# Kernel tuning notes

Hardware: AMD Instinct MI355X
Metric: run time of the kernel (lower is better)

Reference implementation:

```python
import jax, jax.numpy as jnp
import numpy as np

EPS = 1e-5  # BatchNorm eps (torch default)
K = 16      # num_neighbors


def _bn(x, gamma, beta, axes):
    # training-mode BatchNorm (biased variance), channel axis = 1
    mu = x.mean(axes, keepdims=True)
    var = x.var(axes, keepdims=True)
    shp = [1] * x.ndim
    shp[1] = -1
    return (x - mu) * jax.lax.rsqrt(var + EPS) * gamma.reshape(shp) + beta.reshape(shp)


def setup_inputs() -> dict:
    key = jax.random.key(0)
    ks = jax.random.split(key, 6)
    B, C, N, E = 4, 3, 4096, 256
    s = lambda k_, shp, fan: jax.random.normal(k_, shp, jnp.float32) * np.float32(1.0 / np.sqrt(fan))
    return {
        "x": jax.random.normal(ks[0], (B, C, N), jnp.float32),
        "g1": jnp.ones((C,), jnp.float32), "b1": jnp.zeros((C,), jnp.float32),
        "W1": s(ks[1], (E, C), C), "bw1": jnp.zeros((E,), jnp.float32),
        "g2a": jnp.ones((C,), jnp.float32), "b2a": jnp.zeros((C,), jnp.float32),
        "W2a": s(ks[2], (E, C), C),
        "g2b": jnp.ones((E,), jnp.float32), "b2b": jnp.zeros((E,), jnp.float32),
        "W2b": s(ks[3], (E, E), E),
        "Wf": s(ks[4], (E, 2 * E), 2 * E), "bf": jnp.zeros((E,), jnp.float32),
    }


def reference(x, g1, b1, W1, bw1, g2a, b2a, W2a, g2b, b2b, W2b, Wf, bf):
    B, C, N = x.shape
    xn = _bn(x, g1, b1, (0, 2))                               # BatchNorm1d
    point_emb = jnp.einsum('ec,bcn->ben', W1, xn) + bw1[None, :, None]  # conv1 (1x1)
    # dist = -||xi - xj||; torch topk(dist, largest=False) picks the K LARGEST
    # distances. Squared distance is monotone in the norm, so top_k on d2 gives
    # identical indices without materializing [B,3,N,N].
    x2 = jnp.sum(xn * xn, axis=1)                             # [B,N]
    d2 = x2[:, :, None] + x2[:, None, :] - 2.0 * jnp.einsum('bcn,bcm->bnm', xn, xn)
    _, idx = jax.lax.top_k(d2, min(K, N))                     # [B,N,K]
    idx = idx[:, :, 1:]                                       # original loop skips index 0
    gathered = jax.vmap(lambda xb, ib: xb[:, ib])(xn, idx)    # [B,C,N,K-1]
    neigh = gathered - xn[:, :, :, None]                      # edge features
    h = _bn(neigh, g2a, b2a, (0, 2, 3))                       # BatchNorm2d(Cin)
    h = jnp.einsum('ec,bcnk->benk', W2a, h)                   # 1x1 conv, no bias
    h = jax.nn.gelu(_bn(h, g2b, b2b, (0, 2, 3)), approximate=False)
    h = jnp.einsum('fe,benk->bfnk', W2b, h)                   # 1x1 conv, no bias
    neigh_emb = h.max(-1)                                     # max over neighbors
    feat = jnp.concatenate([point_emb, neigh_emb], axis=1)    # [B,2E,N]
    return jnp.einsum('of,bfn->bon', Wf, feat) + bf[None, :, None]
```

## Files before the change

### kernel.cpp

```cpp
#include <hip/hip_runtime.h>
#include <float.h>
#include <math.h>

#define EPS 1e-5f
constexpr int B = 4, C = 3, N = 4096, E = 256;
constexpr int KNN = 15;
constexpr int BN_ = B * N;
constexpr int P = 8;
constexpr int SR  = 264;
constexpr int SRF = 520;

typedef short bf8 __attribute__((ext_vector_type(8)));
typedef float f4  __attribute__((ext_vector_type(4)));

static __device__ __forceinline__ unsigned short f2bf(float f) {
    union { float f; unsigned int u; } v; v.f = f;
    unsigned int r = v.u + 0x7FFFu + ((v.u >> 16) & 1u);
    return (unsigned short)(r >> 16);
}
static __device__ __forceinline__ bf8 ld_bf8(const unsigned short* p) {
    return *(const bf8*)p;
}
static __device__ __forceinline__ float gelu_t(float v) {
    float z = v * fmaf(v * v, 0.07135482f, 1.59576912f);
    float r = __builtin_amdgcn_rcpf(1.f + __expf(z));
    return fmaf(-v, r, v);
}

__global__ void bn1_stats(const float* __restrict__ x, float* __restrict__ bn1) {
    int c = blockIdx.x, t = threadIdx.x;
    float s = 0.f, ss = 0.f;
    for (int i4 = t; i4 < BN_ / 4; i4 += 256) {
        int b = i4 >> 10, n4 = i4 & 1023;
        float4 v = ((const float4*)(x + (b * C + c) * N))[n4];
        s += v.x + v.y + v.z + v.w;
        ss += v.x * v.x + v.y * v.y + v.z * v.z + v.w * v.w;
    }
    __shared__ float rs_[256], rss_[256];
    rs_[t] = s; rss_[t] = ss; __syncthreads();
    for (int w = 128; w > 0; w >>= 1) {
        if (t < w) { rs_[t] += rs_[t + w]; rss_[t] += rss_[t + w]; }
        __syncthreads();
    }
    if (t == 0) {
        float mu = rs_[0] / (float)BN_;
        float var = rss_[0] / (float)BN_ - mu * mu;
        bn1[c] = mu; bn1[3 + c] = rsqrtf(var + EPS);
    }
}

__global__ void compute_xn_cvt(const float* __restrict__ x,
                               const float* __restrict__ g1,
                               const float* __restrict__ b1,
                               const float* __restrict__ bn1,
                               float4* __restrict__ xn4,
                               const float* __restrict__ W2b, const float* __restrict__ Wf,
                               unsigned short* __restrict__ w2b_t, unsigned short* __restrict__ wf_t) {
    int blk = blockIdx.x;
    if (blk < BN_ / 256) {
        int i = blk * 256 + threadIdx.x;
        int b = i >> 12, n = i & (N - 1);
        float v[3];
        #pragma unroll
        for (int c = 0; c < C; c++)
            v[c] = (x[(b * C + c) * N + n] - bn1[c]) * bn1[3 + c] * g1[c] + b1[c];
        float4 o; o.x = v[0]; o.y = v[1]; o.z = v[2];
        o.w = v[0] * v[0] + v[1] * v[1] + v[2] * v[2];
        xn4[i] = o;
        return;
    }
    int ch = (blk - BN_ / 256) * 256 + threadIdx.x;
    if (ch < 8192) {
        int lane = ch & 63, kb = (ch >> 6) & 7, ft16 = ch >> 9;
        int row = ft16 * 16 + (lane & 15);
        int col = kb * 32 + (lane >> 4) * 8;
        #pragma unroll
        for (int j = 0; j < 8; j++)
            w2b_t[ch * 8 + j] = f2bf(W2b[row * 256 + col + j]);
    } else {
        int c2 = ch - 8192;
        int lane = c2 & 63, kb = (c2 >> 6) & 15, ot = c2 >> 10;
        int row = ot * 16 + (lane & 15);
        int col = kb * 32 + (lane >> 4) * 8;
        #pragma unroll
        for (int j = 0; j < 8; j++)
            wf_t[c2 * 8 + j] = f2bf(Wf[row * 512 + col + j]);
    }
}

__global__ void __launch_bounds__(256, 4) knn_kernel(const float4* __restrict__ xn4,
                                                     unsigned short* __restrict__ idxout,
                                                     float* __restrict__ S9) {
    __shared__ float smom[4][15][9];
    int w = threadIdx.x >> 6, lane = threadIdx.x & 63;
    int i = blockIdx.x * 4 + w;
    int b = i >> 12, n = i & (N - 1);
    const float4* xb = xn4 + b * N;
    float4 qv = xb[n];
    float d[64];
    #pragma unroll
    for (int s = 0; s < 64; s++) {
        float4 p = xb[s * 64 + lane];
        d[s] = qv.w + p.w - 2.f * (qv.x * p.x + qv.y * p.y + qv.z * p.z);
    }
    float cm[8];
    #pragma unroll
    for (int c = 0; c < 8; c++) {
        float v = d[c * 8];
        #pragma unroll
        for (int s = 1; s < 8; s++) v = fmaxf(v, d[c * 8 + s]);
        cm[c] = v;
    }
    float bv = cm[0];
    #pragma unroll
    for (int c = 1; c < 8; c++) bv = fmaxf(bv, cm[c]);

    int myj = 0;
    for (int r = 0; r < 16; r++) {
        float wv = bv;
        #pragma unroll
        for (int off = 32; off > 0; off >>= 1)
            wv = fmaxf(wv, __shfl_xor(wv, off));
        unsigned long long msk = __ballot(bv == wv);
        int wl = __ffsll(msk) - 1;
        int gi = 0;
        if (lane == wl) {
            int cstar = 0; bool got = false;
            #pragma unroll
            for (int c = 0; c < 8; c++) {
                bool h = !got && (cm[c] == bv);
                cstar = h ? c : cstar;
                got = got || h;
            }
            int slot = 0;
            #pragma unroll
            for (int c = 0; c < 8; c++) {
                if (c == cstar) {
                    bool g2 = false;
                    #pragma unroll
                    for (int s = 0; s < 8; s++) {
                        bool h = !g2 && (d[c * 8 + s] == bv);
                        slot = h ? (c * 8 + s) : slot;
                        g2 = g2 || h;
                    }
                    #pragma unroll
                    for (int s = 0; s < 8; s++)
                        d[c * 8 + s] = (c * 8 + s == slot) ? -FLT_MAX : d[c * 8 + s];
                    float v = d[c * 8];
                    #pragma unroll
                    for (int s = 1; s < 8; s++) v = fmaxf(v, d[c * 8 + s]);
                    cm[c] = v;
                }
            }
            bv = cm[0];
            #pragma unroll
            for (int c = 1; c < 8; c++) bv = fmaxf(bv, cm[c]);
            gi = slot * 64 + lane;
        }
        int g = __shfl(gi, wl);
        if (lane == r - 1) myj = g;
    }

    bool act = lane < 15;
    if (act) idxout[i * KNN + lane] = (unsigned short)myj;
    float4 pj = xb[act ? myj : n];
    float v0 = pj.x - qv.x, v1 = pj.y - qv.y, v2 = pj.z - qv.z;
    if (act) {
        float* mm = smom[w][lane];
        mm[0] = v0; mm[1] = v1; mm[2] = v2;
        mm[3] = v0 * v0; mm[4] = v1 * v1; mm[5] = v2 * v2;
        mm[6] = v0 * v1; mm[7] = v0 * v2; mm[8] = v1 * v2;
    }
    __syncthreads();
    int t = threadIdx.x;
    if (t < 36) {
        int wsel = t / 9, j = t % 9;
        float a = 0.f;
        #pragma unroll
        for (int u = 0; u < 15; u++) a += smom[wsel][u][j];
        atomicAdd(&S9[((blockIdx.x * 4 + wsel) & 63) * 9 + j], a);
    }
}

__global__ void finalize_stats(const float* __restrict__ S9,
                               const float* __restrict__ g2a, const float* __restrict__ b2a,
                               const float* __restrict__ W2a,
                               const float* __restrict__ g2b, const float* __restrict__ b2b,
                               float* __restrict__ ab, float4* __restrict__ wsb) {
    const float cnt = (float)(BN_ * KNN);
    __shared__ float S[9];
    __shared__ float alpha[3], beta[3], mu[3], Ehh[3][3];
    int t = threadIdx.x;
    if (t < 9) {
        float a = 0.f;
        for (int u = 0; u < 64; u++) a += S9[u * 9 + t];
        S[t] = a;
    }
    __syncthreads();
    if (t == 0) {
        float m[3];
        float s2[3][3];
        s2[0][0] = S[3]; s2[1][1] = S[4]; s2[2][2] = S[5];
        s2[0][1] = s2[1][0] = S[6]; s2[0][2] = s2[2][0] = S[7]; s2[1][2] = s2[2][1] = S[8];
        for (int c = 0; c < 3; c++) {
            m[c] = S[c] / cnt;
            float var = s2[c][c] / cnt - m[c] * m[c];
            alpha[c] = g2a[c] * rsqrtf(var + EPS);
            beta[c]  = b2a[c] - m[c] * alpha[c];
            mu[c] = m[c];
            ab[c] = alpha[c]; ab[3 + c] = beta[c];
        }
        for (int c = 0; c < 3; c++)
            for (int cc = 0; cc < 3; cc++)
                Ehh[c][cc] = alpha[c] * alpha[cc] * (s2[c][cc] / cnt)
                           + alpha[c] * beta[cc] * m[c]
                           + beta[c] * alpha[cc] * m[cc]
                           + beta[c] * beta[cc];
    }
    __syncthreads();
    int e = t;
    float wv[3], Eh[3];
    for (int c = 0; c < 3; c++) { wv[c] = W2a[e * 3 + c]; Eh[c] = alpha[c] * mu[c] + beta[c]; }
    float mean = wv[0] * Eh[0] + wv[1] * Eh[1] + wv[2] * Eh[2];
    float m2 = 0.f;
    for (int c = 0; c < 3; c++)
        for (int cc = 0; cc < 3; cc++) m2 += wv[c] * wv[cc] * Ehh[c][cc];
    float var = m2 - mean * mean;
    float s = g2b[e] * rsqrtf(var + EPS);
    float4 o;
    o.x = wv[0] * s; o.y = wv[1] * s; o.z = wv[2] * s; o.w = b2b[e] - mean * s;
    wsb[e] = o;
}

__global__ void __launch_bounds__(512, 4) fused_final(
        const float4* __restrict__ xn4, const unsigned short* __restrict__ idx,
        const float* __restrict__ ab,
        const float4* __restrict__ wsb,
        const unsigned short* __restrict__ w2b_t,
        const float* __restrict__ W1, const float* __restrict__ bw1,
        const unsigned short* __restrict__ wf_t, const float* __restrict__ bfv,
        float* __restrict__ out) {
    __shared__ __align__(16) unsigned short hh_bf[128 * SR];
    __shared__ __align__(16) unsigned short feat_bf[8 * SRF];
    __shared__ __align__(16) float4 hhat4[P][16];
    int i0 = blockIdx.x * P;
    int t = threadIdx.x;
    int b = i0 >> 12, n0 = i0 & (N - 1);
    const float4* xb = xn4 + b * N;

    if (t < P * KNN) {
        int p = t / KNN, k = t % KNN;
        int j = idx[(i0 + p) * KNN + k];
        float4 pj = xb[j];
        float4 pn = xb[n0 + p];
        float4 h;
        h.x = ab[0] * (pj.x - pn.x) + ab[3];
        h.y = ab[1] * (pj.y - pn.y) + ab[4];
        h.z = ab[2] * (pj.z - pn.z) + ab[5];
        h.w = 0.f;
        hhat4[p][k] = h;
    }
    __syncthreads();

    {
        int e = t & 255;
        int ph = t >> 8;
        float4 w4 = wsb[e];
        #pragma unroll
        for (int pp = 0; pp < 4; pp++) {
            int p = ph * 4 + pp;
            float g0 = 0.f;
            #pragma unroll
            for (int k = 0; k < KNN; k++) {
                float4 hv = hhat4[p][k];
                float v = fmaf(w4.x, hv.x, fmaf(w4.y, hv.y, fmaf(w4.z, hv.z, w4.w)));
                float g = gelu_t(v);
                hh_bf[(16 * p + k) * SR + e] = f2bf(g);
                if (k == 0) g0 = g;
            }
            hh_bf[(16 * p + 15) * SR + e] = f2bf(g0);
            float4 pv = xb[n0 + p];
            feat_bf[p * SRF + e] = f2bf(bw1[e] + W1[e * 3] * pv.x
                       + W1[e * 3 + 1] * pv.y + W1[e * 3 + 2] * pv.z);
        }
    }
    __syncthreads();

    int w = t >> 6, lane = t & 63;
    int m = lane & 15, q = lane >> 4;

    {
        #pragma unroll
        for (int f = 0; f < 2; f++) {
            int ft = w * 2 + f;
            bf8 a[8];
            #pragma unroll
            for (int kb = 0; kb < 8; kb++)
                a[kb] = ld_bf8(w2b_t + ft * 4096 + kb * 512 + lane * 8);
            #pragma unroll 1
            for (int pr = 0; pr < 4; pr++) {
                bf8 hfr[2][8];
                #pragma unroll
                for (int pi = 0; pi < 2; pi++)
                    #pragma unroll
                    for (int kb = 0; kb < 8; kb++)
                        hfr[pi][kb] = ld_bf8(&hh_bf[(16 * (pr * 2 + pi) + m) * SR + kb * 32 + q * 8]);
                #pragma unroll
                for (int pi = 0; pi < 2; pi++) {
                    f4 acc = {0.f, 0.f, 0.f, 0.f};
                    #pragma unroll
                    for (int kb = 0; kb < 8; kb++)
                        acc = __builtin_amdgcn_mfma_f32_16x16x32_bf16(hfr[pi][kb], a[kb], acc, 0, 0, 0);
                    float mx = fmaxf(fmaxf(acc[0], acc[1]), fmaxf(acc[2], acc[3]));
                    mx = fmaxf(mx, __shfl_xor(mx, 16));
                    mx = fmaxf(mx, __shfl_xor(mx, 32));
                    if (lane < 16)
                        feat_bf[(pr * 2 + pi) * SRF + E + ft * 16 + lane] = f2bf(mx);
                }
            }
        }
    }
    __syncthreads();

    {
        bf8 fb[16];
        #pragma unroll
        for (int kb = 0; kb < 16; kb++)
            fb[kb] = ld_bf8(&feat_bf[(m & 7) * SRF + kb * 32 + q * 8]);
        #pragma unroll
        for (int o2 = 0; o2 < 2; o2++) {
            int ot = w * 2 + o2;
            f4 acc = {0.f, 0.f, 0.f, 0.f};
            #pragma unroll
            for (int kb = 0; kb < 16; kb++) {
                bf8 a = ld_bf8(wf_t + ot * 8192 + kb * 512 + lane * 8);
                acc = __builtin_amdgcn_mfma_f32_16x16x32_bf16(a, fb[kb], acc, 0, 0, 0);
            }
            if (m < P) {
                int o0 = ot * 16 + 4 * q;
                out[(b * E + o0 + 0) * N + n0 + m] = acc[0] + bfv[o0 + 0];
                out[(b * E + o0 + 1) * N + n0 + m] = acc[1] + bfv[o0 + 1];
                out[(b * E + o0 + 2) * N + n0 + m] = acc[2] + bfv[o0 + 2];
                out[(b * E + o0 + 3) * N + n0 + m] = acc[3] + bfv[o0 + 3];
            }
        }
    }
}

extern "C" void kernel_launch(void* const* d_in, const int* in_sizes, int n_in,
                              void* d_out, int out_size, void* d_ws, size_t ws_size,
                              hipStream_t stream) {
    (void)in_sizes; (void)n_in; (void)out_size; (void)ws_size;
    const float* x   = (const float*)d_in[0];
    const float* g1  = (const float*)d_in[1];
    const float* b1  = (const float*)d_in[2];
    const float* W1  = (const float*)d_in[3];
    const float* bw1 = (const float*)d_in[4];
    const float* g2a = (const float*)d_in[5];
    const float* b2a = (const float*)d_in[6];
    const float* W2a = (const float*)d_in[7];
    const float* g2b = (const float*)d_in[8];
    const float* b2b = (const float*)d_in[9];
    const float* W2b = (const float*)d_in[10];
    const float* Wf  = (const float*)d_in[11];
    const float* bfv = (const float*)d_in[12];
    float* out = (float*)d_out;

    char* ws = (char*)d_ws;
    size_t off = 0;
    auto alloc = [&](size_t bytes) { size_t o = off; off = (off + bytes + 255) & ~(size_t)255; return o; };
    float4* xn4           = (float4*)(ws + alloc(sizeof(float4) * BN_));
    unsigned short* idx   = (unsigned short*)(ws + alloc(sizeof(unsigned short) * BN_ * KNN));
    float* bn1            = (float*)(ws + alloc(sizeof(float) * 8));
    float* S9             = (float*)(ws + alloc(sizeof(float) * 64 * 9));
    float* ab             = (float*)(ws + alloc(sizeof(float) * 8));
    float4* wsb           = (float4*)(ws + alloc(sizeof(float4) * E));
    unsigned short* w2bt  = (unsigned short*)(ws + alloc(sizeof(unsigned short) * E * E));
    unsigned short* wft   = (unsigned short*)(ws + alloc(sizeof(unsigned short) * E * 2 * E));

    hipMemsetAsync(S9, 0, sizeof(float) * 64 * 9, stream);

    bn1_stats<<<C, 256, 0, stream>>>(x, bn1);
    compute_xn_cvt<<<BN_ / 256 + (8192 + 16384) / 256, 256, 0, stream>>>(
        x, g1, b1, bn1, xn4, W2b, Wf, w2bt, wft);
    knn_kernel<<<BN_ / 4, 256, 0, stream>>>(xn4, idx, S9);
    finalize_stats<<<1, 256, 0, stream>>>(S9, g2a, b2a, W2a, g2b, b2b, ab, wsb);
    fused_final<<<BN_ / P, 512, 0, stream>>>(xn4, idx, ab, wsb, w2bt, W1, bw1, wft, bfv, out);
}
```

Baseline: 247.1 us.

## Halve hh LDS buffer by processing points in two groups, pack bf16 stores

```diff
diff --git a/kernel.cpp b/kernel.cpp
--- a/kernel.cpp
+++ b/kernel.cpp
@@ -17,6 +17,11 @@
     union { float f; unsigned int u; } v; v.f = f;
     unsigned int r = v.u + 0x7FFFu + ((v.u >> 16) & 1u);
     return (unsigned short)(r >> 16);
+}
+static __device__ __forceinline__ unsigned int pkbf(float a, float b) {
+    unsigned int r;
+    asm("v_cvt_pk_bf16_f32 %0, %1, %2" : "=v"(r) : "v"(a), "v"(b));
+    return r;
 }
 static __device__ __forceinline__ bf8 ld_bf8(const unsigned short* p) {
     return *(const bf8*)p;
@@ -232,7 +237,7 @@
     wsb[e] = o;
 }
 
-__global__ void __launch_bounds__(512, 4) fused_final(
+__global__ void __launch_bounds__(512, 6) fused_final(
         const float4* __restrict__ xn4, const unsigned short* __restrict__ idx,
         const float* __restrict__ ab,
         const float4* __restrict__ wsb,
@@ -240,7 +245,7 @@
         const float* __restrict__ W1, const float* __restrict__ bw1,
         const unsigned short* __restrict__ wf_t, const float* __restrict__ bfv,
         float* __restrict__ out) {
-    __shared__ __align__(16) unsigned short hh_bf[128 * SR];
+    __shared__ __align__(16) unsigned short hh_bf[64 * SR];
     __shared__ __align__(16) unsigned short feat_bf[8 * SRF];
     __shared__ __align__(16) float4 hhat4[P][16];
     int i0 = blockIdx.x * P;
@@ -262,65 +267,70 @@
     }
     __syncthreads();
 
-    {
-        int e = t & 255;
-        int ph = t >> 8;
-        float4 w4 = wsb[e];
-        #pragma unroll
-        for (int pp = 0; pp < 4; pp++) {
-            int p = ph * 4 + pp;
-            float g0 = 0.f;
+    int w = t >> 6, lane = t & 63;
+    int m = lane & 15, q = lane >> 4;
+
+    #pragma unroll 1
+    for (int pg = 0; pg < 2; pg++) {
+        {
+            int ep = t & 127;
+            int pq = t >> 7;
+            int p  = pg * 4 + pq;
+            float4 wA = wsb[2 * ep];
+            float4 wB = wsb[2 * ep + 1];
+            float g0A = 0.f, g0B = 0.f;
             #pragma unroll
             for (int k = 0; k < KNN; k++) {
                 float4 hv = hhat4[p][k];
-                float v = fmaf(w4.x, hv.x, fmaf(w4.y, hv.y, fmaf(w4.z, hv.z, w4.w)));
-                float g = gelu_t(v);
-                hh_bf[(16 * p + k) * SR + e] = f2bf(g);
-                if (k == 0) g0 = g;
-            }
-            hh_bf[(16 * p + 15) * SR + e] = f2bf(g0);
+                float vA = fmaf(wA.x, hv.x, fmaf(wA.y, hv.y, fmaf(wA.z, hv.z, wA.w)));
+                float vB = fmaf(wB.x, hv.x, fmaf(wB.y, hv.y, fmaf(wB.z, hv.z, wB.w)));
+                float gA = gelu_t(vA), gB = gelu_t(vB);
+                *(unsigned int*)&hh_bf[(16 * pq + k) * SR + 2 * ep] = pkbf(gA, gB);
+                if (k == 0) { g0A = gA; g0B = gB; }
+            }
+            *(unsigned int*)&hh_bf[(16 * pq + 15) * SR + 2 * ep] = pkbf(g0A, g0B);
             float4 pv = xb[n0 + p];
-            feat_bf[p * SRF + e] = f2bf(bw1[e] + W1[e * 3] * pv.x
-                       + W1[e * 3 + 1] * pv.y + W1[e * 3 + 2] * pv.z);
-        }
-    }
-    __syncthreads();
-
-    int w = t >> 6, lane = t & 63;
-    int m = lane & 15, q = lane >> 4;
-
-    {
-        #pragma unroll
-        for (int f = 0; f < 2; f++) {
-            int ft = w * 2 + f;
-            bf8 a[8];
-            #pragma unroll
-            for (int kb = 0; kb < 8; kb++)
-                a[kb] = ld_bf8(w2b_t + ft * 4096 + kb * 512 + lane * 8);
-            #pragma unroll 1
-            for (int pr = 0; pr < 4; pr++) {
-                bf8 hfr[2][8];
+            float peA = bw1[2 * ep] + W1[(2 * ep) * 3] * pv.x
+                      + W1[(2 * ep) * 3 + 1] * pv.y + W1[(2 * ep) * 3 + 2] * pv.z;
+            float peB = bw1[2 * ep + 1] + W1[(2 * ep + 1) * 3] * pv.x
+                      + W1[(2 * ep + 1) * 3 + 1] * pv.y + W1[(2 * ep + 1) * 3 + 2] * pv.z;
+            *(unsigned int*)&feat_bf[p * SRF + 2 * ep] = pkbf(peA, peB);
+        }
+        __syncthreads();
+
+        {
+            #pragma unroll
+            for (int f = 0; f < 2; f++) {
+                int ft = w * 2 + f;
+                bf8 a[8];
                 #pragma unroll
-                for (int pi = 0; pi < 2; pi++)
-                    #pragma unroll
-                    for (int kb = 0; kb < 8; kb++)
-                        hfr[pi][kb] = ld_bf8(&hh_bf[(16 * (pr * 2 + pi) + m) * SR + kb * 32 + q * 8]);
-                #pragma unroll
-                for (int pi = 0; pi < 2; pi++) {
-                    f4 acc = {0.f, 0.f, 0.f, 0.f};
-                    #pragma unroll
-                    for (int kb = 0; kb < 8; kb++)
-                        acc = __builtin_amdgcn_mfma_f32_16x16x32_bf16(hfr[pi][kb], a[kb], acc, 0, 0, 0);
-                    float mx = fmaxf(fmaxf(acc[0], acc[1]), fmaxf(acc[2], acc[3]));
-                    mx = fmaxf(mx, __shfl_xor(mx, 16));
-                    mx = fmaxf(mx, __shfl_xor(mx, 32));
-                    if (lane < 16)
-                        feat_bf[(pr * 2 + pi) * SRF + E + ft * 16 + lane] = f2bf(mx);
+                for (int kb = 0; kb < 8; kb++)
+                    a[kb] = ld_bf8(w2b_t + ft * 4096 + kb * 512 + lane * 8);
+                #pragma unroll 1
+                for (int pr = 0; pr < 2; pr++) {
+                    bf8 hfr[2][8];
+                    #pragma unroll
+                    for (int pi = 0; pi < 2; pi++)
+                        #pragma unroll
+                        for (int kb = 0; kb < 8; kb++)
+                            hfr[pi][kb] = ld_bf8(&hh_bf[(16 * (pr * 2 + pi) + m) * SR + kb * 32 + q * 8]);
+                    #pragma unroll
+                    for (int pi = 0; pi < 2; pi++) {
+                        f4 acc = {0.f, 0.f, 0.f, 0.f};
+                        #pragma unroll
+                        for (int kb = 0; kb < 8; kb++)
+                            acc = __builtin_amdgcn_mfma_f32_16x16x32_bf16(hfr[pi][kb], a[kb], acc, 0, 0, 0);
+                        float mx = fmaxf(fmaxf(acc[0], acc[1]), fmaxf(acc[2], acc[3]));
+                        mx = fmaxf(mx, __shfl_xor(mx, 16));
+                        mx = fmaxf(mx, __shfl_xor(mx, 32));
+                        if (lane < 16)
+                            feat_bf[(pg * 4 + pr * 2 + pi) * SRF + E + ft * 16 + lane] = f2bf(mx);
+                    }
                 }
             }
         }
-    }
-    __syncthreads();
+        __syncthreads();
+    }
 
     {
         bf8 fb[16];
```

Result: slower. 303.3 us (+22.8%).

## Stage KNN candidate points in shared memory and use DPP wave max

Applied to the files above, without the earlier changes.

```diff
diff --git a/kernel.cpp b/kernel.cpp
--- a/kernel.cpp
+++ b/kernel.cpp
@@ -25,6 +25,22 @@
     float z = v * fmaf(v * v, 0.07135482f, 1.59576912f);
     float r = __builtin_amdgcn_rcpf(1.f + __expf(z));
     return fmaf(-v, r, v);
+}
+
+template <int CTRL>
+static __device__ __forceinline__ float dppmax(float x) {
+    int xi = __float_as_int(x);
+    int yi = __builtin_amdgcn_update_dpp(xi, xi, CTRL, 0xF, 0xF, false);
+    return fmaxf(x, __int_as_float(yi));
+}
+static __device__ __forceinline__ float wave_max_bcast(float x) {
+    x = dppmax<0x111>(x);
+    x = dppmax<0x112>(x);
+    x = dppmax<0x114>(x);
+    x = dppmax<0x118>(x);
+    x = dppmax<0x142>(x);
+    x = dppmax<0x143>(x);
+    return __int_as_float(__builtin_amdgcn_readlane(__float_as_int(x), 63));
 }
 
 __global__ void bn1_stats(const float* __restrict__ x, float* __restrict__ bn1) {
@@ -92,6 +108,7 @@
                                                      unsigned short* __restrict__ idxout,
                                                      float* __restrict__ S9) {
     __shared__ float smom[4][15][9];
+    __shared__ __align__(16) float4 pts[1024];
     int w = threadIdx.x >> 6, lane = threadIdx.x & 63;
     int i = blockIdx.x * 4 + w;
     int b = i >> 12, n = i & (N - 1);
@@ -99,9 +116,17 @@
     float4 qv = xb[n];
     float d[64];
     #pragma unroll
-    for (int s = 0; s < 64; s++) {
-        float4 p = xb[s * 64 + lane];
-        d[s] = qv.w + p.w - 2.f * (qv.x * p.x + qv.y * p.y + qv.z * p.z);
+    for (int ch = 0; ch < 4; ch++) {
+        if (ch) __syncthreads();
+        #pragma unroll
+        for (int u = 0; u < 4; u++)
+            pts[u * 256 + threadIdx.x] = xb[ch * 1024 + u * 256 + threadIdx.x];
+        __syncthreads();
+        #pragma unroll
+        for (int j = 0; j < 16; j++) {
+            float4 p = pts[j * 64 + lane];
+            d[ch * 16 + j] = qv.w + p.w - 2.f * (qv.x * p.x + qv.y * p.y + qv.z * p.z);
+        }
     }
     float cm[8];
     #pragma unroll
@@ -117,10 +142,7 @@
 
     int myj = 0;
     for (int r = 0; r < 16; r++) {
-        float wv = bv;
-        #pragma unroll
-        for (int off = 32; off > 0; off >>= 1)
-            wv = fmaxf(wv, __shfl_xor(wv, off));
+        float wv = wave_max_bcast(bv);
         unsigned long long msk = __ballot(bv == wv);
         int wl = __ffsll(msk) - 1;
         int gi = 0;
```

Measured after the change: 235.7 us. 1.05x faster.
